# Optimization experiments

Measured on AMD Instinct MI355X. Metric: run time of the kernel, lower is better.

Reference implementation:

```python
import jax, jax.numpy as jnp
import numpy as np

N, D, K_FRAC = 4096, 256, 0.5
EPS = 1e-5  # BatchNorm1d default eps


def setup_inputs() -> dict:
    key = jax.random.key(0)
    kg, kh, kw = jax.random.split(key, 3)
    # sparse binary adjacency with self-loops so all degrees > 0 (pow(D,-1) finite)
    g = (jax.random.uniform(kg, (N, N)) < 0.004).astype(jnp.float32)
    g = jnp.maximum(g, jnp.eye(N, dtype=jnp.float32))
    h = jax.random.normal(kh, (N, D), dtype=jnp.float32)
    return {
        "g": g,
        "h": h,
        "gamma": jnp.ones((D,), jnp.float32),
        "beta": jnp.zeros((D,), jnp.float32),
        "w_proj": jax.random.normal(kw, (D, 1), dtype=jnp.float32) / np.sqrt(D),
        "b_proj": jnp.zeros((1,), jnp.float32),
        "sigma1": jnp.array([0.2], jnp.float32),
    }


def reference(g, h, gamma, beta, w_proj, b_proj, sigma1):
    # BatchNorm1d in training mode: batch statistics over the node axis
    mu = h.mean(0)
    var = h.var(0)  # biased variance, as torch uses for normalization
    h = (h - mu) / jnp.sqrt(var + EPS) * gamma + beta

    deg = g.sum(1)                               # [N] == Z2
    agg = (g @ h) / deg[:, None]                 # diag(D^-1) @ (g @ h), no NxN diag materialized
    Z1 = jnp.abs(h - agg).sum(1)                 # [N]
    pl = jax.nn.sigmoid(Z1 + deg)
    Z3 = (agg @ w_proj + b_proj)[:, 0]           # proj(Z3).squeeze()
    pg = jax.nn.softmax(Z3)                      # 1-D softmax (dim 0)
    pt = jax.nn.sigmoid(pl + pg)
    pf = jax.nn.sigmoid((h @ w_proj + b_proj)[:, 0])
    scores = sigma1[0] * pt + (1.0 - sigma1[0]) * pf

    # top_k_graph
    k = max(2, int(K_FRAC * N))
    _, idx = jax.lax.top_k(scores, k)            # [k]
    h_att = scores[:, None] * h                  # score-weighted features
    un_g = (g != 0).astype(jnp.float32)
    two_hop = ((un_g @ un_g) != 0).astype(jnp.float32)  # binarized 2-hop adjacency
    a_hat = two_hop[idx, :]                      # [k, N] row gather
    new_h = a_hat @ h_att                        # [k, D]
    g_new = a_hat[:, idx]                        # [k, k] column gather
    # norm_g: torch broadcast divides COLUMN j by row-sum degrees[j]
    g_new = g_new / g_new.sum(1)
    return g_new, new_h, idx
```

## Files before the change

### kernel.cpp

```cpp
#include <hip/hip_runtime.h>
#include <math.h>

#define NN 4096
#define DD 256
#define KK 2048
#define NW 64

__device__ __forceinline__ int build_list(const unsigned long long* __restrict__ B, int r,
                                          int l, int* cols, int cap) {
    unsigned long long word = B[(size_t)r * NW + l];
    int pc = __popcll(word);
    int off = pc;
    for (int d = 1; d < 64; d <<= 1) {
        int n = __shfl_up(off, d);
        if (l >= d) off += n;
    }
    int total = __shfl(off, 63);
    int base = off - pc;
    while (word) {
        int b = (int)__ffsll(word) - 1;
        word &= word - 1;
        if (base < cap) cols[base] = l * 64 + b;
        ++base;
    }
    return total;
}

__global__ void k_pre(const float* __restrict__ h, const float* __restrict__ g,
                      double* __restrict__ psum, double* __restrict__ psq,
                      unsigned long long* __restrict__ B) {
    int blk = blockIdx.x;
    int t = threadIdx.x;
    if (blk < 64) {
        int d = t;
        int r0 = blk * 64;
        double s0=0,s1=0,s2=0,s3=0,q0=0,q1=0,q2=0,q3=0;
        for (int k = 0; k < 64; k += 4) {
            double x0 = (double)h[(size_t)(r0+k+0) * DD + d];
            double x1 = (double)h[(size_t)(r0+k+1) * DD + d];
            double x2 = (double)h[(size_t)(r0+k+2) * DD + d];
            double x3 = (double)h[(size_t)(r0+k+3) * DD + d];
            s0 += x0; q0 += x0*x0;
            s1 += x1; q1 += x1*x1;
            s2 += x2; q2 += x2*x2;
            s3 += x3; q3 += x3*x3;
        }
        psum[blk * DD + d] = (s0+s1)+(s2+s3);
        psq [blk * DD + d] = (q0+q1)+(q2+q3);
    } else {
        int i = blk - 64;
        int q = t >> 6, l = t & 63;
        const float4* g4 = (const float4*)(g + (size_t)i * NN);
        for (int wi = 0; wi < 4; ++wi) {
            float4 v = g4[q * 256 + wi * 64 + l];
            unsigned int nib = (unsigned int)(v.x != 0.f)
                             | ((unsigned int)(v.y != 0.f) << 1)
                             | ((unsigned int)(v.z != 0.f) << 2)
                             | ((unsigned int)(v.w != 0.f) << 3);
            unsigned long long word = (unsigned long long)nib << (4 * (l & 15));
            unsigned int lo = (unsigned int)word, hi = (unsigned int)(word >> 32);
            for (int s = 1; s < 16; s <<= 1) {
                lo |= __shfl_xor(lo, s, 16);
                hi |= __shfl_xor(hi, s, 16);
            }
            if ((l & 15) == 0)
                B[(size_t)i * NW + 16 * q + 4 * wi + (l >> 4)] =
                    ((unsigned long long)hi << 32) | lo;
        }
    }
}

__global__ void k_stats_final(const double* __restrict__ psum, const double* __restrict__ psq,
                              double* __restrict__ mu, double* __restrict__ rstd) {
    __shared__ double rs[4][DD];
    __shared__ double rq[4][DD];
    int t = threadIdx.x;
    int d = t & (DD - 1);
    int q = t >> 8;
    double s0=0,s1=0,q0=0,q1=0;
    int b0 = q * 16;
    for (int k = 0; k < 16; k += 2) {
        s0 += psum[(b0+k)   * DD + d];
        s1 += psum[(b0+k+1) * DD + d];
        q0 += psq [(b0+k)   * DD + d];
        q1 += psq [(b0+k+1) * DD + d];
    }
    rs[q][d] = s0 + s1;
    rq[q][d] = q0 + q1;
    __syncthreads();
    if (q == 0) {
        double S  = (rs[0][d]+rs[1][d]) + (rs[2][d]+rs[3][d]);
        double Q  = (rq[0][d]+rq[1][d]) + (rq[2][d]+rq[3][d]);
        double m  = S / (double)NN;
        double var = Q / (double)NN - m * m;
        mu[d]   = m;
        rstd[d] = 1.0 / sqrt(var + 1e-5);
    }
}

__global__ void k_main(const float* __restrict__ h, const double* __restrict__ mu,
                       const double* __restrict__ rstd, const float* __restrict__ gamma,
                       const float* __restrict__ beta, const unsigned long long* __restrict__ Bm,
                       const float* __restrict__ w, const float* __restrict__ bp,
                       float* __restrict__ hn, double* __restrict__ zpf,
                       unsigned long long* __restrict__ T, double* __restrict__ Z1,
                       double* __restrict__ Z3, int* __restrict__ degi) {
    __shared__ int cols[4][136];
    int blk = blockIdx.x;
    int t = threadIdx.x;
    int wv = t >> 6, l = t & 63;
    if (blk < 1024) {
        int r = blk * 4 + wv;
        int cnt = build_list(Bm, r, l, cols[wv], 128);
        if (cnt > 128) cnt = 128;
        const float4* h4 = (const float4*)h;
        double s0=0,s1=0,s2=0,s3=0,u0=0,u1=0,u2=0,u3=0;
        int j = 0;
        for (; j + 1 < cnt; j += 2) {
            float4 v0 = h4[(size_t)cols[wv][j]     * 64 + l];
            float4 v1 = h4[(size_t)cols[wv][j + 1] * 64 + l];
            s0 += (double)v0.x; s1 += (double)v0.y; s2 += (double)v0.z; s3 += (double)v0.w;
            u0 += (double)v1.x; u1 += (double)v1.y; u2 += (double)v1.z; u3 += (double)v1.w;
        }
        if (j < cnt) {
            float4 v0 = h4[(size_t)cols[wv][j] * 64 + l];
            s0 += (double)v0.x; s1 += (double)v0.y; s2 += (double)v0.z; s3 += (double)v0.w;
        }
        s0 += u0; s1 += u1; s2 += u2; s3 += u3;
        const double2* mu2 = (const double2*)mu;
        const double2* rs2 = (const double2*)rstd;
        const float4*  ga4 = (const float4*)gamma;
        const float4*  be4 = (const float4*)beta;
        const float4*  w4  = (const float4*)w;
        double2 mA = mu2[2*l], mB = mu2[2*l+1];
        double2 rA = rs2[2*l], rB = rs2[2*l+1];
        float4 ga = ga4[l], be = be4[l], wl = w4[l];
        double inv = 1.0 / (double)cnt;
        double g0 = (s0 * inv - mA.x) * rA.x * (double)ga.x + (double)be.x;
        double g1 = (s1 * inv - mA.y) * rA.y * (double)ga.y + (double)be.y;
        double g2 = (s2 * inv - mB.x) * rB.x * (double)ga.z + (double)be.z;
        double g3 = (s3 * inv - mB.y) * rB.y * (double)ga.w + (double)be.w;
        float4 hv = h4[(size_t)r * 64 + l];
        double h0 = ((double)hv.x - mA.x) * rA.x * (double)ga.x + (double)be.x;
        double h1 = ((double)hv.y - mA.y) * rA.y * (double)ga.y + (double)be.y;
        double h2 = ((double)hv.z - mB.x) * rB.x * (double)ga.z + (double)be.z;
        double h3 = ((double)hv.w - mB.y) * rB.y * (double)ga.w + (double)be.w;
        float4 o = { (float)h0, (float)h1, (float)h2, (float)h3 };
        ((float4*)hn)[(size_t)r * 64 + l] = o;
        double z1p = (fabs(h0 - g0) + fabs(h1 - g1)) + (fabs(h2 - g2) + fabs(h3 - g3));
        double z3p = (g0 * (double)wl.x + g1 * (double)wl.y)
                   + (g2 * (double)wl.z + g3 * (double)wl.w);
        double zfp = (h0 * (double)wl.x + h1 * (double)wl.y)
                   + (h2 * (double)wl.z + h3 * (double)wl.w);
        for (int off = 32; off > 0; off >>= 1) {
            z1p += __shfl_down(z1p, off);
            z3p += __shfl_down(z3p, off);
            zfp += __shfl_down(zfp, off);
        }
        if (l == 0) {
            Z1[r] = z1p;
            Z3[r] = z3p + (double)bp[0];
            zpf[r] = zfp + (double)bp[0];
            degi[r] = cnt;
        }
    } else {
        int r = (blk - 1024) * 4 + wv;
        int cnt = build_list(Bm, r, l, cols[wv], 128);
        if (cnt > 128) cnt = 128;
        unsigned long long a0 = 0ull, a1 = 0ull;
        int j = 0;
        for (; j + 1 < cnt; j += 2) {
            a0 |= Bm[(size_t)cols[wv][j]     * NW + l];
            a1 |= Bm[(size_t)cols[wv][j + 1] * NW + l];
        }
        if (j < cnt) a0 |= Bm[(size_t)cols[wv][j] * NW + l];
        T[(size_t)r * NW + l] = a0 | a1;
    }
}

__global__ void k_scorekeys(const double* __restrict__ Z1, const double* __restrict__ Z3,
                            const double* __restrict__ zpf, const int* __restrict__ degi,
                            const float* __restrict__ sigma1, float* __restrict__ scores,
                            unsigned long long* __restrict__ keys) {
    __shared__ double red[256];
    int t = threadIdx.x;
    double mx = -1e300;
    for (int k = 0; k < 16; ++k) mx = fmax(mx, Z3[t + 256 * k]);
    red[t] = mx;
    __syncthreads();
    for (int s = 128; s > 0; s >>= 1) {
        if (t < s) red[t] = fmax(red[t], red[t + s]);
        __syncthreads();
    }
    double M = red[0];
    __syncthreads();
    double se = 0.0;
    for (int k = 0; k < 16; ++k) se += exp(Z3[t + 256 * k] - M);
    red[t] = se;
    __syncthreads();
    for (int s = 128; s > 0; s >>= 1) {
        if (t < s) red[t] += red[t + s];
        __syncthreads();
    }
    double sum = red[0];
    int i = blockIdx.x * 256 + t;
    double s1 = (double)sigma1[0];
    double pg = exp(Z3[i] - M) / sum;
    double pl = 1.0 / (1.0 + exp(-(Z1[i] + (double)degi[i])));
    double pt = 1.0 / (1.0 + exp(-(pl + pg)));
    double pf = 1.0 / (1.0 + exp(-zpf[i]));
    float sc = (float)(s1 * pt + (1.0 - s1) * pf);
    scores[i] = sc;
    unsigned int b2 = __float_as_uint(sc);
    unsigned int ka = (b2 & 0x80000000u) ? ~b2 : (b2 ^ 0x80000000u);
    keys[i] = ((unsigned long long)(~ka) << 32) | (unsigned int)i;
}

__global__ void k_rank(const unsigned long long* __restrict__ keys, int* __restrict__ idx_int,
                       float* __restrict__ out_idx) {
    __shared__ unsigned long long Kl[NN];
    int t = threadIdx.x;
    for (int i = t; i < NN; i += 256) Kl[i] = keys[i];
    __syncthreads();
    int il = t >> 4, sub = t & 15;
    int i = blockIdx.x * 16 + il;
    unsigned long long ki = Kl[i];
    int c0 = 0, c1 = 0, c2 = 0, c3 = 0;
    for (int jj = 0; jj < 256; jj += 4) {
        int j = sub + (jj << 4);
        c0 += (Kl[j]      < ki) ? 1 : 0;
        c1 += (Kl[j + 16] < ki) ? 1 : 0;
        c2 += (Kl[j + 32] < ki) ? 1 : 0;
        c3 += (Kl[j + 48] < ki) ? 1 : 0;
    }
    int cnt = (c0 + c1) + (c2 + c3);
    for (int off = 8; off > 0; off >>= 1) cnt += __shfl_down(cnt, off, 16);
    if (sub == 0 && cnt < KK) {
        idx_int[cnt] = i;
        out_idx[cnt] = (float)i;
    }
}

__global__ void k_rowsum(const unsigned long long* __restrict__ T, const int* __restrict__ idx_int,
                         float* __restrict__ inv_rs) {
    __shared__ unsigned long long Sl[NW];
    int t = threadIdx.x;
    Sl[t] = 0ull;
    for (int j = t; j < KK; j += 64) {
        int ii = idx_int[j];
        atomicOr(&Sl[ii >> 6], 1ull << (ii & 63));
    }
    int j = blockIdx.x * 64 + t;
    int r = idx_int[j];
    const unsigned long long* Tr = T + (size_t)r * NW;
    int c0 = 0, c1 = 0, c2 = 0, c3 = 0;
    for (int w = 0; w < NW; w += 4) {
        c0 += __popcll(Tr[w]     & Sl[w]);
        c1 += __popcll(Tr[w + 1] & Sl[w + 1]);
        c2 += __popcll(Tr[w + 2] & Sl[w + 2]);
        c3 += __popcll(Tr[w + 3] & Sl[w + 3]);
    }
    inv_rs[j] = 1.0f / (float)((c0 + c1) + (c2 + c3));
}

__global__ void k_out(const unsigned long long* __restrict__ T, const int* __restrict__ idx_int,
                      const float* __restrict__ inv_rs, const float* __restrict__ scores,
                      const float* __restrict__ hn, float* __restrict__ out_gnew,
                      float* __restrict__ out_newh) {
    __shared__ unsigned long long Tl[NW];
    __shared__ int cols[2048];
    __shared__ int s_cnt;
    __shared__ float4 red[4][64];
    int blk = blockIdx.x;
    int t = threadIdx.x;
    if (blk < KK) {
        int r = blk;
        if (t < NW) Tl[t] = T[(size_t)idx_int[r] * NW + t];
        __syncthreads();
        const int4*   idx4 = (const int4*)idx_int;
        const float4* irs4 = (const float4*)inv_rs;
        float4* out4 = (float4*)(out_gnew + (size_t)r * KK);
        for (int c4 = t; c4 < KK / 4; c4 += 256) {
            int4 jc = idx4[c4];
            float4 iv = irs4[c4];
            float4 o;
            o.x = ((Tl[jc.x >> 6] >> (jc.x & 63)) & 1ull) ? iv.x : 0.0f;
            o.y = ((Tl[jc.y >> 6] >> (jc.y & 63)) & 1ull) ? iv.y : 0.0f;
            o.z = ((Tl[jc.z >> 6] >> (jc.z & 63)) & 1ull) ? iv.z : 0.0f;
            o.w = ((Tl[jc.w >> 6] >> (jc.w & 63)) & 1ull) ? iv.w : 0.0f;
            out4[c4] = o;
        }
    } else {
        int r = blk - KK;
        int wv = t >> 6, l = t & 63;
        if (t < 64) {
            int total = build_list(T, idx_int[r], t, cols, 2048);
            if (t == 63) s_cnt = total;
        }
        __syncthreads();
        int cnt = s_cnt < 2048 ? s_cnt : 2048;
        const float4* hn4 = (const float4*)hn;
        float4 a0 = {0,0,0,0}, a1 = {0,0,0,0}, a2 = {0,0,0,0}, a3 = {0,0,0,0};
        int j = wv;
        for (; j + 12 < cnt; j += 16) {
            int c0 = cols[j], c1 = cols[j + 4], c2 = cols[j + 8], c3 = cols[j + 12];
            float s0 = scores[c0], s1 = scores[c1], s2 = scores[c2], s3 = scores[c3];
            float4 v0 = hn4[(size_t)c0 * 64 + l];
            float4 v1 = hn4[(size_t)c1 * 64 + l];
            float4 v2 = hn4[(size_t)c2 * 64 + l];
            float4 v3 = hn4[(size_t)c3 * 64 + l];
            a0.x = fmaf(s0, v0.x, a0.x); a0.y = fmaf(s0, v0.y, a0.y);
            a0.z = fmaf(s0, v0.z, a0.z); a0.w = fmaf(s0, v0.w, a0.w);
            a1.x = fmaf(s1, v1.x, a1.x); a1.y = fmaf(s1, v1.y, a1.y);
            a1.z = fmaf(s1, v1.z, a1.z); a1.w = fmaf(s1, v1.w, a1.w);
            a2.x = fmaf(s2, v2.x, a2.x); a2.y = fmaf(s2, v2.y, a2.y);
            a2.z = fmaf(s2, v2.z, a2.z); a2.w = fmaf(s2, v2.w, a2.w);
            a3.x = fmaf(s3, v3.x, a3.x); a3.y = fmaf(s3, v3.y, a3.y);
            a3.z = fmaf(s3, v3.z, a3.z); a3.w = fmaf(s3, v3.w, a3.w);
        }
        for (; j < cnt; j += 4) {
            int c0 = cols[j];
            float s0 = scores[c0];
            float4 v0 = hn4[(size_t)c0 * 64 + l];
            a0.x = fmaf(s0, v0.x, a0.x); a0.y = fmaf(s0, v0.y, a0.y);
            a0.z = fmaf(s0, v0.z, a0.z); a0.w = fmaf(s0, v0.w, a0.w);
        }
        float4 acc;
        acc.x = (a0.x + a1.x) + (a2.x + a3.x);
        acc.y = (a0.y + a1.y) + (a2.y + a3.y);
        acc.z = (a0.z + a1.z) + (a2.z + a3.z);
        acc.w = (a0.w + a1.w) + (a2.w + a3.w);
        red[wv][l] = acc;
        __syncthreads();
        if (t < 64) {
            float4 r0 = red[0][t], r1 = red[1][t], r2 = red[2][t], r3 = red[3][t];
            float4 o;
            o.x = (r0.x + r1.x) + (r2.x + r3.x);
            o.y = (r0.y + r1.y) + (r2.y + r3.y);
            o.z = (r0.z + r1.z) + (r2.z + r3.z);
            o.w = (r0.w + r1.w) + (r2.w + r3.w);
            ((float4*)(out_newh + (size_t)r * DD))[t] = o;
        }
    }
}

extern "C" void kernel_launch(void* const* d_in, const int* in_sizes, int n_in,
                              void* d_out, int out_size, void* d_ws, size_t ws_size,
                              hipStream_t stream) {
    const float* g      = (const float*)d_in[0];
    const float* h      = (const float*)d_in[1];
    const float* gamma  = (const float*)d_in[2];
    const float* beta   = (const float*)d_in[3];
    const float* w_proj = (const float*)d_in[4];
    const float* b_proj = (const float*)d_in[5];
    const float* sigma1 = (const float*)d_in[6];

    char* p = (char*)d_ws;
    auto alloc = [&](size_t bytes) -> void* {
        void* q = (void*)p;
        p += (bytes + 255) & ~(size_t)255;
        return q;
    };
    double* mu      = (double*)alloc(DD * 8);
    double* rstd    = (double*)alloc(DD * 8);
    double* psum    = (double*)alloc(64 * DD * 8);
    double* psq     = (double*)alloc(64 * DD * 8);
    double* zpf     = (double*)alloc(NN * 8);
    double* Z1      = (double*)alloc(NN * 8);
    double* Z3      = (double*)alloc(NN * 8);
    int*    degi    = (int*)alloc(NN * 4);
    float*  scores  = (float*)alloc(NN * 4);
    unsigned long long* keys = (unsigned long long*)alloc(NN * 8);
    int*    idx_int = (int*)alloc(KK * 4);
    float*  inv_rs  = (float*)alloc(KK * 4);
    unsigned long long* B = (unsigned long long*)alloc((size_t)NN * NW * 8);
    unsigned long long* T = (unsigned long long*)alloc((size_t)NN * NW * 8);
    float*  hn      = (float*)alloc((size_t)NN * DD * 4);

    float* out_gnew = (float*)d_out;
    float* out_newh = out_gnew + (size_t)KK * KK;
    float* out_idx  = out_newh + (size_t)KK * DD;

    hipLaunchKernelGGL(k_pre,         dim3(64 + NN), dim3(256),  0, stream, h, g, psum, psq, B);
    hipLaunchKernelGGL(k_stats_final, dim3(1),       dim3(1024), 0, stream, psum, psq, mu, rstd);
    hipLaunchKernelGGL(k_main,        dim3(2048),    dim3(256),  0, stream, h, mu, rstd, gamma, beta, B, w_proj, b_proj, hn, zpf, T, Z1, Z3, degi);
    hipLaunchKernelGGL(k_scorekeys,   dim3(16),      dim3(256),  0, stream, Z1, Z3, zpf, degi, sigma1, scores, keys);
    hipLaunchKernelGGL(k_rank,        dim3(256),     dim3(256),  0, stream, keys, idx_int, out_idx);
    hipLaunchKernelGGL(k_rowsum,      dim3(32),      dim3(64),   0, stream, T, idx_int, inv_rs);
    hipLaunchKernelGGL(k_out,         dim3(2 * KK),  dim3(256),  0, stream, T, idx_int, inv_rs, scores, hn, out_gnew, out_newh);
}
```

Before: 179.7 us.

## Fuse post-preprocessing stages into one cooperative persistent kernel with grid syncs

Replaces the six kernels after k_pre (stats finalize, main, score/keys, rank, rowsum, output) with a single cooperative kernel of 512 blocks that separates phases with grid.sync. Every block redundantly computes the softmax and scores and ranks 8 rows from a shared-memory key array, which removes the separate key buffer and several launch gaps. The output phase now gives one row per wave and no longer splits a row across 4 waves with a cross-wave reduction. In exchange it adds grid-wide barrier costs and redundant score computation in every block, and it holds a 32KB shared union that can limit occupancy.

```diff
diff --git a/kernel.cpp b/kernel.cpp
--- a/kernel.cpp
+++ b/kernel.cpp
@@ -1,5 +1,8 @@
 #include <hip/hip_runtime.h>
+#include <hip/hip_cooperative_groups.h>
 #include <math.h>
+
+namespace cg = cooperative_groups;
 
 #define NN 4096
 #define DD 256
@@ -70,63 +73,66 @@
     }
 }
 
-__global__ void k_stats_final(const double* __restrict__ psum, const double* __restrict__ psq,
-                              double* __restrict__ mu, double* __restrict__ rstd) {
-    __shared__ double rs[4][DD];
-    __shared__ double rq[4][DD];
-    int t = threadIdx.x;
-    int d = t & (DD - 1);
-    int q = t >> 8;
-    double s0=0,s1=0,q0=0,q1=0;
-    int b0 = q * 16;
-    for (int k = 0; k < 16; k += 2) {
-        s0 += psum[(b0+k)   * DD + d];
-        s1 += psum[(b0+k+1) * DD + d];
-        q0 += psq [(b0+k)   * DD + d];
-        q1 += psq [(b0+k+1) * DD + d];
-    }
-    rs[q][d] = s0 + s1;
-    rq[q][d] = q0 + q1;
-    __syncthreads();
-    if (q == 0) {
-        double S  = (rs[0][d]+rs[1][d]) + (rs[2][d]+rs[3][d]);
-        double Q  = (rq[0][d]+rq[1][d]) + (rq[2][d]+rq[3][d]);
-        double m  = S / (double)NN;
-        double var = Q / (double)NN - m * m;
-        mu[d]   = m;
-        rstd[d] = 1.0 / sqrt(var + 1e-5);
-    }
-}
-
-__global__ void k_main(const float* __restrict__ h, const double* __restrict__ mu,
-                       const double* __restrict__ rstd, const float* __restrict__ gamma,
-                       const float* __restrict__ beta, const unsigned long long* __restrict__ Bm,
-                       const float* __restrict__ w, const float* __restrict__ bp,
-                       float* __restrict__ hn, double* __restrict__ zpf,
-                       unsigned long long* __restrict__ T, double* __restrict__ Z1,
-                       double* __restrict__ Z3, int* __restrict__ degi) {
-    __shared__ int cols[4][136];
-    int blk = blockIdx.x;
-    int t = threadIdx.x;
-    int wv = t >> 6, l = t & 63;
-    if (blk < 1024) {
-        int r = blk * 4 + wv;
-        int cnt = build_list(Bm, r, l, cols[wv], 128);
-        if (cnt > 128) cnt = 128;
-        const float4* h4 = (const float4*)h;
-        double s0=0,s1=0,s2=0,s3=0,u0=0,u1=0,u2=0,u3=0;
-        int j = 0;
-        for (; j + 1 < cnt; j += 2) {
-            float4 v0 = h4[(size_t)cols[wv][j]     * 64 + l];
-            float4 v1 = h4[(size_t)cols[wv][j + 1] * 64 + l];
-            s0 += (double)v0.x; s1 += (double)v0.y; s2 += (double)v0.z; s3 += (double)v0.w;
-            u0 += (double)v1.x; u1 += (double)v1.y; u2 += (double)v1.z; u3 += (double)v1.w;
-        }
-        if (j < cnt) {
-            float4 v0 = h4[(size_t)cols[wv][j] * 64 + l];
-            s0 += (double)v0.x; s1 += (double)v0.y; s2 += (double)v0.z; s3 += (double)v0.w;
-        }
-        s0 += u0; s1 += u1; s2 += u2; s3 += u3;
+__global__ __launch_bounds__(256, 2) void k_coop(
+    const float* __restrict__ h, const float* __restrict__ gamma,
+    const float* __restrict__ beta, const float* __restrict__ w,
+    const float* __restrict__ bp, const float* __restrict__ sigma1,
+    const double* __restrict__ psum, const double* __restrict__ psq,
+    const unsigned long long* __restrict__ B,
+    double* __restrict__ mu, double* __restrict__ rstd,
+    float* __restrict__ hn, double* __restrict__ zpf,
+    unsigned long long* __restrict__ T, double* __restrict__ Z1,
+    double* __restrict__ Z3, int* __restrict__ degi,
+    float* __restrict__ scores, int* __restrict__ idx_int,
+    float* __restrict__ inv_rs, float* __restrict__ out_gnew,
+    float* __restrict__ out_newh, float* __restrict__ out_idx)
+{
+    cg::grid_group grid = cg::this_grid();
+    __shared__ union U {
+        unsigned long long Kl[NN];
+        int cols4[4][2048];
+        unsigned long long Sl[NW];
+    } sh;
+    __shared__ double red[256];
+    __shared__ unsigned long long Tl4[4][NW];
+    const int blk = blockIdx.x;
+    const int t = threadIdx.x;
+    const int wv = t >> 6, l = t & 63;
+    const int gw = blk * 4 + wv;
+
+    if (blk < 64) {
+        int d = blk * 4 + wv;
+        double s = psum[l * DD + d];
+        double q = psq [l * DD + d];
+        for (int off = 32; off > 0; off >>= 1) {
+            s += __shfl_down(s, off);
+            q += __shfl_down(q, off);
+        }
+        if (l == 0) {
+            double m = s / (double)NN;
+            double var = q / (double)NN - m * m;
+            mu[d]   = m;
+            rstd[d] = 1.0 / sqrt(var + 1e-5);
+        }
+    }
+    grid.sync();
+
+    {
+        int* cols = sh.cols4[wv];
+        for (int pass = 0; pass < 2; ++pass) {
+            int r = gw + pass * 2048;
+            int cnt = build_list(B, r, l, cols, 128);
+            if (cnt > 128) cnt = 128;
+            unsigned long long a0 = 0ull, a1 = 0ull;
+            int j = 0;
+            for (; j + 1 < cnt; j += 2) {
+                a0 |= B[(size_t)cols[j]     * NW + l];
+                a1 |= B[(size_t)cols[j + 1] * NW + l];
+            }
+            if (j < cnt) a0 |= B[(size_t)cols[j] * NW + l];
+            T[(size_t)r * NW + l] = a0 | a1;
+        }
+        const float4*  h4  = (const float4*)h;
         const double2* mu2 = (const double2*)mu;
         const double2* rs2 = (const double2*)rstd;
         const float4*  ga4 = (const float4*)gamma;
@@ -135,175 +141,153 @@
         double2 mA = mu2[2*l], mB = mu2[2*l+1];
         double2 rA = rs2[2*l], rB = rs2[2*l+1];
         float4 ga = ga4[l], be = be4[l], wl = w4[l];
-        double inv = 1.0 / (double)cnt;
-        double g0 = (s0 * inv - mA.x) * rA.x * (double)ga.x + (double)be.x;
-        double g1 = (s1 * inv - mA.y) * rA.y * (double)ga.y + (double)be.y;
-        double g2 = (s2 * inv - mB.x) * rB.x * (double)ga.z + (double)be.z;
-        double g3 = (s3 * inv - mB.y) * rB.y * (double)ga.w + (double)be.w;
-        float4 hv = h4[(size_t)r * 64 + l];
-        double h0 = ((double)hv.x - mA.x) * rA.x * (double)ga.x + (double)be.x;
-        double h1 = ((double)hv.y - mA.y) * rA.y * (double)ga.y + (double)be.y;
-        double h2 = ((double)hv.z - mB.x) * rB.x * (double)ga.z + (double)be.z;
-        double h3 = ((double)hv.w - mB.y) * rB.y * (double)ga.w + (double)be.w;
-        float4 o = { (float)h0, (float)h1, (float)h2, (float)h3 };
-        ((float4*)hn)[(size_t)r * 64 + l] = o;
-        double z1p = (fabs(h0 - g0) + fabs(h1 - g1)) + (fabs(h2 - g2) + fabs(h3 - g3));
-        double z3p = (g0 * (double)wl.x + g1 * (double)wl.y)
-                   + (g2 * (double)wl.z + g3 * (double)wl.w);
-        double zfp = (h0 * (double)wl.x + h1 * (double)wl.y)
-                   + (h2 * (double)wl.z + h3 * (double)wl.w);
-        for (int off = 32; off > 0; off >>= 1) {
-            z1p += __shfl_down(z1p, off);
-            z3p += __shfl_down(z3p, off);
-            zfp += __shfl_down(zfp, off);
-        }
-        if (l == 0) {
-            Z1[r] = z1p;
-            Z3[r] = z3p + (double)bp[0];
-            zpf[r] = zfp + (double)bp[0];
-            degi[r] = cnt;
-        }
-    } else {
-        int r = (blk - 1024) * 4 + wv;
-        int cnt = build_list(Bm, r, l, cols[wv], 128);
-        if (cnt > 128) cnt = 128;
-        unsigned long long a0 = 0ull, a1 = 0ull;
-        int j = 0;
-        for (; j + 1 < cnt; j += 2) {
-            a0 |= Bm[(size_t)cols[wv][j]     * NW + l];
-            a1 |= Bm[(size_t)cols[wv][j + 1] * NW + l];
-        }
-        if (j < cnt) a0 |= Bm[(size_t)cols[wv][j] * NW + l];
-        T[(size_t)r * NW + l] = a0 | a1;
-    }
-}
-
-__global__ void k_scorekeys(const double* __restrict__ Z1, const double* __restrict__ Z3,
-                            const double* __restrict__ zpf, const int* __restrict__ degi,
-                            const float* __restrict__ sigma1, float* __restrict__ scores,
-                            unsigned long long* __restrict__ keys) {
-    __shared__ double red[256];
-    int t = threadIdx.x;
-    double mx = -1e300;
-    for (int k = 0; k < 16; ++k) mx = fmax(mx, Z3[t + 256 * k]);
-    red[t] = mx;
-    __syncthreads();
-    for (int s = 128; s > 0; s >>= 1) {
-        if (t < s) red[t] = fmax(red[t], red[t + s]);
-        __syncthreads();
-    }
-    double M = red[0];
-    __syncthreads();
-    double se = 0.0;
-    for (int k = 0; k < 16; ++k) se += exp(Z3[t + 256 * k] - M);
-    red[t] = se;
-    __syncthreads();
-    for (int s = 128; s > 0; s >>= 1) {
-        if (t < s) red[t] += red[t + s];
-        __syncthreads();
-    }
-    double sum = red[0];
-    int i = blockIdx.x * 256 + t;
-    double s1 = (double)sigma1[0];
-    double pg = exp(Z3[i] - M) / sum;
-    double pl = 1.0 / (1.0 + exp(-(Z1[i] + (double)degi[i])));
-    double pt = 1.0 / (1.0 + exp(-(pl + pg)));
-    double pf = 1.0 / (1.0 + exp(-zpf[i]));
-    float sc = (float)(s1 * pt + (1.0 - s1) * pf);
-    scores[i] = sc;
-    unsigned int b2 = __float_as_uint(sc);
-    unsigned int ka = (b2 & 0x80000000u) ? ~b2 : (b2 ^ 0x80000000u);
-    keys[i] = ((unsigned long long)(~ka) << 32) | (unsigned int)i;
-}
-
-__global__ void k_rank(const unsigned long long* __restrict__ keys, int* __restrict__ idx_int,
-                       float* __restrict__ out_idx) {
-    __shared__ unsigned long long Kl[NN];
-    int t = threadIdx.x;
-    for (int i = t; i < NN; i += 256) Kl[i] = keys[i];
-    __syncthreads();
-    int il = t >> 4, sub = t & 15;
-    int i = blockIdx.x * 16 + il;
-    unsigned long long ki = Kl[i];
-    int c0 = 0, c1 = 0, c2 = 0, c3 = 0;
-    for (int jj = 0; jj < 256; jj += 4) {
-        int j = sub + (jj << 4);
-        c0 += (Kl[j]      < ki) ? 1 : 0;
-        c1 += (Kl[j + 16] < ki) ? 1 : 0;
-        c2 += (Kl[j + 32] < ki) ? 1 : 0;
-        c3 += (Kl[j + 48] < ki) ? 1 : 0;
-    }
-    int cnt = (c0 + c1) + (c2 + c3);
-    for (int off = 8; off > 0; off >>= 1) cnt += __shfl_down(cnt, off, 16);
-    if (sub == 0 && cnt < KK) {
-        idx_int[cnt] = i;
-        out_idx[cnt] = (float)i;
-    }
-}
-
-__global__ void k_rowsum(const unsigned long long* __restrict__ T, const int* __restrict__ idx_int,
-                         float* __restrict__ inv_rs) {
-    __shared__ unsigned long long Sl[NW];
-    int t = threadIdx.x;
-    Sl[t] = 0ull;
-    for (int j = t; j < KK; j += 64) {
-        int ii = idx_int[j];
-        atomicOr(&Sl[ii >> 6], 1ull << (ii & 63));
-    }
-    int j = blockIdx.x * 64 + t;
-    int r = idx_int[j];
-    const unsigned long long* Tr = T + (size_t)r * NW;
-    int c0 = 0, c1 = 0, c2 = 0, c3 = 0;
-    for (int w = 0; w < NW; w += 4) {
-        c0 += __popcll(Tr[w]     & Sl[w]);
-        c1 += __popcll(Tr[w + 1] & Sl[w + 1]);
-        c2 += __popcll(Tr[w + 2] & Sl[w + 2]);
-        c3 += __popcll(Tr[w + 3] & Sl[w + 3]);
-    }
-    inv_rs[j] = 1.0f / (float)((c0 + c1) + (c2 + c3));
-}
-
-__global__ void k_out(const unsigned long long* __restrict__ T, const int* __restrict__ idx_int,
-                      const float* __restrict__ inv_rs, const float* __restrict__ scores,
-                      const float* __restrict__ hn, float* __restrict__ out_gnew,
-                      float* __restrict__ out_newh) {
-    __shared__ unsigned long long Tl[NW];
-    __shared__ int cols[2048];
-    __shared__ int s_cnt;
-    __shared__ float4 red[4][64];
-    int blk = blockIdx.x;
-    int t = threadIdx.x;
-    if (blk < KK) {
-        int r = blk;
-        if (t < NW) Tl[t] = T[(size_t)idx_int[r] * NW + t];
+        for (int pass = 0; pass < 2; ++pass) {
+            int r = gw + pass * 2048;
+            int cnt = build_list(B, r, l, cols, 128);
+            if (cnt > 128) cnt = 128;
+            double s0=0,s1=0,s2=0,s3=0,u0=0,u1=0,u2=0,u3=0;
+            int j = 0;
+            for (; j + 1 < cnt; j += 2) {
+                float4 v0 = h4[(size_t)cols[j]     * 64 + l];
+                float4 v1 = h4[(size_t)cols[j + 1] * 64 + l];
+                s0 += (double)v0.x; s1 += (double)v0.y; s2 += (double)v0.z; s3 += (double)v0.w;
+                u0 += (double)v1.x; u1 += (double)v1.y; u2 += (double)v1.z; u3 += (double)v1.w;
+            }
+            if (j < cnt) {
+                float4 v0 = h4[(size_t)cols[j] * 64 + l];
+                s0 += (double)v0.x; s1 += (double)v0.y; s2 += (double)v0.z; s3 += (double)v0.w;
+            }
+            s0 += u0; s1 += u1; s2 += u2; s3 += u3;
+            double inv = 1.0 / (double)cnt;
+            double g0 = (s0 * inv - mA.x) * rA.x * (double)ga.x + (double)be.x;
+            double g1 = (s1 * inv - mA.y) * rA.y * (double)ga.y + (double)be.y;
+            double g2 = (s2 * inv - mB.x) * rB.x * (double)ga.z + (double)be.z;
+            double g3 = (s3 * inv - mB.y) * rB.y * (double)ga.w + (double)be.w;
+            float4 hv = h4[(size_t)r * 64 + l];
+            double h0 = ((double)hv.x - mA.x) * rA.x * (double)ga.x + (double)be.x;
+            double h1 = ((double)hv.y - mA.y) * rA.y * (double)ga.y + (double)be.y;
+            double h2 = ((double)hv.z - mB.x) * rB.x * (double)ga.z + (double)be.z;
+            double h3 = ((double)hv.w - mB.y) * rB.y * (double)ga.w + (double)be.w;
+            float4 o = { (float)h0, (float)h1, (float)h2, (float)h3 };
+            ((float4*)hn)[(size_t)r * 64 + l] = o;
+            double z1p = (fabs(h0 - g0) + fabs(h1 - g1)) + (fabs(h2 - g2) + fabs(h3 - g3));
+            double z3p = (g0 * (double)wl.x + g1 * (double)wl.y)
+                       + (g2 * (double)wl.z + g3 * (double)wl.w);
+            double zfp = (h0 * (double)wl.x + h1 * (double)wl.y)
+                       + (h2 * (double)wl.z + h3 * (double)wl.w);
+            for (int off = 32; off > 0; off >>= 1) {
+                z1p += __shfl_down(z1p, off);
+                z3p += __shfl_down(z3p, off);
+                zfp += __shfl_down(zfp, off);
+            }
+            if (l == 0) {
+                Z1[r] = z1p;
+                Z3[r] = z3p + (double)bp[0];
+                zpf[r] = zfp + (double)bp[0];
+                degi[r] = cnt;
+            }
+        }
+    }
+    grid.sync();
+
+    {
+        double mx = -1e300;
+        for (int k = 0; k < 16; ++k) mx = fmax(mx, Z3[t + 256 * k]);
+        red[t] = mx;
+        __syncthreads();
+        for (int s = 128; s > 0; s >>= 1) {
+            if (t < s) red[t] = fmax(red[t], red[t + s]);
+            __syncthreads();
+        }
+        double M = red[0];
+        __syncthreads();
+        double se = 0.0;
+        for (int k = 0; k < 16; ++k) se += exp(Z3[t + 256 * k] - M);
+        red[t] = se;
+        __syncthreads();
+        for (int s = 128; s > 0; s >>= 1) {
+            if (t < s) red[t] += red[t + s];
+            __syncthreads();
+        }
+        double sum = red[0];
+        double s1 = (double)sigma1[0];
+        for (int k = 0; k < 16; ++k) {
+            int i = t + 256 * k;
+            double pg = exp(Z3[i] - M) / sum;
+            double pl = 1.0 / (1.0 + exp(-(Z1[i] + (double)degi[i])));
+            double pt = 1.0 / (1.0 + exp(-(pl + pg)));
+            double pf = 1.0 / (1.0 + exp(-zpf[i]));
+            float sc = (float)(s1 * pt + (1.0 - s1) * pf);
+            if ((i >> 3) == blk) scores[i] = sc;
+            unsigned int b2 = __float_as_uint(sc);
+            unsigned int ka = (b2 & 0x80000000u) ? ~b2 : (b2 ^ 0x80000000u);
+            sh.Kl[i] = ((unsigned long long)(~ka) << 32) | (unsigned int)i;
+        }
+        __syncthreads();
+        int il = t >> 5, sub = t & 31;
+        int i = blk * 8 + il;
+        unsigned long long ki = sh.Kl[i];
+        int c0 = 0, c1 = 0, c2 = 0, c3 = 0;
+        for (int jj = 0; jj < NN; jj += 128) {
+            int j = sub + jj;
+            c0 += (sh.Kl[j]      < ki) ? 1 : 0;
+            c1 += (sh.Kl[j + 32] < ki) ? 1 : 0;
+            c2 += (sh.Kl[j + 64] < ki) ? 1 : 0;
+            c3 += (sh.Kl[j + 96] < ki) ? 1 : 0;
+        }
+        int cnt = (c0 + c1) + (c2 + c3);
+        for (int off = 16; off > 0; off >>= 1) cnt += __shfl_down(cnt, off, 32);
+        if (sub == 0 && cnt < KK) {
+            idx_int[cnt] = i;
+            out_idx[cnt] = (float)i;
+        }
+    }
+    grid.sync();
+
+    {
+        if (t < NW) sh.Sl[t] = 0ull;
+        __syncthreads();
+        for (int j = t; j < KK; j += 256) {
+            int ii = idx_int[j];
+            atomicOr(&sh.Sl[ii >> 6], 1ull << (ii & 63));
+        }
+        __syncthreads();
+        int j = blk * 4 + wv;
+        int r = idx_int[j];
+        int c = __popcll(T[(size_t)r * NW + l] & sh.Sl[l]);
+        for (int off = 32; off > 0; off >>= 1) c += __shfl_down(c, off);
+        if (l == 0) inv_rs[j] = 1.0f / (float)c;
+    }
+    grid.sync();
+
+    {
+        int r0 = blk * 4;
+        Tl4[wv][l] = T[(size_t)idx_int[r0 + wv] * NW + l];
         __syncthreads();
         const int4*   idx4 = (const int4*)idx_int;
         const float4* irs4 = (const float4*)inv_rs;
-        float4* out4 = (float4*)(out_gnew + (size_t)r * KK);
         for (int c4 = t; c4 < KK / 4; c4 += 256) {
             int4 jc = idx4[c4];
             float4 iv = irs4[c4];
-            float4 o;
-            o.x = ((Tl[jc.x >> 6] >> (jc.x & 63)) & 1ull) ? iv.x : 0.0f;
-            o.y = ((Tl[jc.y >> 6] >> (jc.y & 63)) & 1ull) ? iv.y : 0.0f;
-            o.z = ((Tl[jc.z >> 6] >> (jc.z & 63)) & 1ull) ? iv.z : 0.0f;
-            o.w = ((Tl[jc.w >> 6] >> (jc.w & 63)) & 1ull) ? iv.w : 0.0f;
-            out4[c4] = o;
-        }
-    } else {
-        int r = blk - KK;
-        int wv = t >> 6, l = t & 63;
-        if (t < 64) {
-            int total = build_list(T, idx_int[r], t, cols, 2048);
-            if (t == 63) s_cnt = total;
-        }
-        __syncthreads();
-        int cnt = s_cnt < 2048 ? s_cnt : 2048;
+            #pragma unroll
+            for (int k = 0; k < 4; ++k) {
+                float4 o;
+                o.x = ((Tl4[k][jc.x >> 6] >> (jc.x & 63)) & 1ull) ? iv.x : 0.0f;
+                o.y = ((Tl4[k][jc.y >> 6] >> (jc.y & 63)) & 1ull) ? iv.y : 0.0f;
+                o.z = ((Tl4[k][jc.z >> 6] >> (jc.z & 63)) & 1ull) ? iv.z : 0.0f;
+                o.w = ((Tl4[k][jc.w >> 6] >> (jc.w & 63)) & 1ull) ? iv.w : 0.0f;
+                ((float4*)(out_gnew + (size_t)(r0 + k) * KK))[c4] = o;
+            }
+        }
+        int r = r0 + wv;
+        int* cols = sh.cols4[wv];
+        int cnt = build_list(T, idx_int[r], l, cols, 2048);
+        if (cnt > 2048) cnt = 2048;
         const float4* hn4 = (const float4*)hn;
         float4 a0 = {0,0,0,0}, a1 = {0,0,0,0}, a2 = {0,0,0,0}, a3 = {0,0,0,0};
-        int j = wv;
-        for (; j + 12 < cnt; j += 16) {
-            int c0 = cols[j], c1 = cols[j + 4], c2 = cols[j + 8], c3 = cols[j + 12];
+        int j = 0;
+        for (; j + 3 < cnt; j += 4) {
+            int c0 = cols[j], c1 = cols[j+1], c2 = cols[j+2], c3 = cols[j+3];
             float s0 = scores[c0], s1 = scores[c1], s2 = scores[c2], s3 = scores[c3];
             float4 v0 = hn4[(size_t)c0 * 64 + l];
             float4 v1 = hn4[(size_t)c1 * 64 + l];
@@ -318,7 +302,7 @@
             a3.x = fmaf(s3, v3.x, a3.x); a3.y = fmaf(s3, v3.y, a3.y);
             a3.z = fmaf(s3, v3.z, a3.z); a3.w = fmaf(s3, v3.w, a3.w);
         }
-        for (; j < cnt; j += 4) {
+        for (; j < cnt; ++j) {
             int c0 = cols[j];
             float s0 = scores[c0];
             float4 v0 = hn4[(size_t)c0 * 64 + l];
@@ -330,17 +314,7 @@
         acc.y = (a0.y + a1.y) + (a2.y + a3.y);
         acc.z = (a0.z + a1.z) + (a2.z + a3.z);
         acc.w = (a0.w + a1.w) + (a2.w + a3.w);
-        red[wv][l] = acc;
-        __syncthreads();
-        if (t < 64) {
-            float4 r0 = red[0][t], r1 = red[1][t], r2 = red[2][t], r3 = red[3][t];
-            float4 o;
-            o.x = (r0.x + r1.x) + (r2.x + r3.x);
-            o.y = (r0.y + r1.y) + (r2.y + r3.y);
-            o.z = (r0.z + r1.z) + (r2.z + r3.z);
-            o.w = (r0.w + r1.w) + (r2.w + r3.w);
-            ((float4*)(out_newh + (size_t)r * DD))[t] = o;
-        }
+        ((float4*)(out_newh + (size_t)r * DD))[l] = acc;
     }
 }
 
@@ -370,7 +344,6 @@
     double* Z3      = (double*)alloc(NN * 8);
     int*    degi    = (int*)alloc(NN * 4);
     float*  scores  = (float*)alloc(NN * 4);
-    unsigned long long* keys = (unsigned long long*)alloc(NN * 8);
     int*    idx_int = (int*)alloc(KK * 4);
     float*  inv_rs  = (float*)alloc(KK * 4);
     unsigned long long* B = (unsigned long long*)alloc((size_t)NN * NW * 8);
@@ -381,11 +354,14 @@
     float* out_newh = out_gnew + (size_t)KK * KK;
     float* out_idx  = out_newh + (size_t)KK * DD;
 
-    hipLaunchKernelGGL(k_pre,         dim3(64 + NN), dim3(256),  0, stream, h, g, psum, psq, B);
-    hipLaunchKernelGGL(k_stats_final, dim3(1),       dim3(1024), 0, stream, psum, psq, mu, rstd);
-    hipLaunchKernelGGL(k_main,        dim3(2048),    dim3(256),  0, stream, h, mu, rstd, gamma, beta, B, w_proj, b_proj, hn, zpf, T, Z1, Z3, degi);
-    hipLaunchKernelGGL(k_scorekeys,   dim3(16),      dim3(256),  0, stream, Z1, Z3, zpf, degi, sigma1, scores, keys);
-    hipLaunchKernelGGL(k_rank,        dim3(256),     dim3(256),  0, stream, keys, idx_int, out_idx);
-    hipLaunchKernelGGL(k_rowsum,      dim3(32),      dim3(64),   0, stream, T, idx_int, inv_rs);
-    hipLaunchKernelGGL(k_out,         dim3(2 * KK),  dim3(256),  0, stream, T, idx_int, inv_rs, scores, hn, out_gnew, out_newh);
+    hipLaunchKernelGGL(k_pre, dim3(64 + NN), dim3(256), 0, stream, h, g, psum, psq, B);
+
+    void* cargs[] = {
+        (void*)&h, (void*)&gamma, (void*)&beta, (void*)&w_proj, (void*)&b_proj,
+        (void*)&sigma1, (void*)&psum, (void*)&psq, (void*)&B, (void*)&mu, (void*)&rstd,
+        (void*)&hn, (void*)&zpf, (void*)&T, (void*)&Z1, (void*)&Z3, (void*)&degi,
+        (void*)&scores, (void*)&idx_int, (void*)&inv_rs,
+        (void*)&out_gnew, (void*)&out_newh, (void*)&out_idx
+    };
+    hipLaunchCooperativeKernel((void*)k_coop, dim3(512), dim3(256), cargs, 0, stream);
 }
```

Result: slower. 409.5 us (+127.8%).
